# Kernel tuning notes

Hardware: AMD Instinct MI355X
Metric: run time of the kernel (lower is better)

Reference implementation:

```python
import jax, jax.numpy as jnp
import numpy as np

NUM_HEADS = 8
KEY_DIM = 512  # d_gain = 1/sqrt(key_dim) in the original (NOT per-head dim)
MASK_FILL = -1000000.0


def setup_inputs() -> dict:
    key = jax.random.key(0)
    ks = jax.random.split(key, 6)
    N, Tq, Tk, D, U = 8, 1024, 1024, 512, 512
    query = jax.random.normal(ks[0], (N, Tq, D), dtype=jnp.float32)
    key_t = jax.random.normal(ks[1], (N, Tk, D), dtype=jnp.float32)
    key_mask = jax.random.randint(ks[2], (N, Tk), 0, 2).astype(bool)
    Wq = jax.random.normal(ks[3], (D, U), dtype=jnp.float32) / np.sqrt(D)
    Wk = jax.random.normal(ks[4], (D, U), dtype=jnp.float32) / np.sqrt(D)
    Wv = jax.random.normal(ks[5], (D, U), dtype=jnp.float32) / np.sqrt(D)
    return {"query": query, "key": key_t, "key_mask": key_mask,
            "Wq": Wq, "Wk": Wk, "Wv": Wv}


def reference(query, key, key_mask, Wq, Wk, Wv):
    N, Tq, _ = query.shape
    Tk = key.shape[1]
    U = Wq.shape[1]
    h = NUM_HEADS
    d = U // h
    scale = 1.0 / (KEY_DIM ** 0.5)

    # projections then split heads: [N,T,U] -> [h,N,T,d]
    q = (query @ Wq).reshape(N, Tq, h, d).transpose(2, 0, 1, 3)
    k = (key @ Wk).reshape(N, Tk, h, d).transpose(2, 0, 1, 3)
    v = (key @ Wv).reshape(N, Tk, h, d).transpose(2, 0, 1, 3)

    scores = scale * jnp.einsum('hnqd,hnkd->hnqk', q, k)
    scores = jnp.where(key_mask[None, :, None, :], scores, MASK_FILL)
    attn = jax.nn.softmax(scores, axis=3)
    out = jnp.einsum('hnqk,hnkd->hnqd', attn, v)
    # merge heads: [h,N,Tq,d] -> [N,Tq,h*d]
    return out.transpose(1, 2, 0, 3).reshape(N, Tq, U)
```

## Files before the change

kernel.cpp:

```cpp
#include <hip/hip_runtime.h>
#include <hip/hip_bf16.h>

typedef unsigned short u16;
typedef __attribute__((ext_vector_type(8))) short short8;
typedef __attribute__((ext_vector_type(4))) short short4v;
typedef __attribute__((ext_vector_type(4))) float f32x4;

#define NB 8
#define TT 1024
#define DD 512
#define UU 512
#define HH 8
#define DH 64
#define SCALE 0.044194173824159216f
#define LOG2E 1.4426950408889634f
#define MASK_FILL_2 -1442695.0f

__device__ __forceinline__ float ld_flex(const void* p, long i, bool f32) {
  if (f32) return ((const float*)p)[i];
  unsigned int u = (unsigned int)(((const u16*)p)[i]) << 16;
  return __uint_as_float(u);
}

__device__ __forceinline__ u16 f32_to_bf16(float f) {
  unsigned int u = __float_as_uint(f);
  unsigned int r = (u + 0x7FFFu + ((u >> 16) & 1u)) >> 16;
  return (u16)r;
}

__device__ __forceinline__ float ex2(float x) {
#if __has_builtin(__builtin_amdgcn_exp2f)
  return __builtin_amdgcn_exp2f(x);
#else
  return __expf(x * 0.6931471805599453f);
#endif
}

__device__ __forceinline__ unsigned int pk_bf16(float a, float b) {
  union { __hip_bfloat162 h2; unsigned int u; } c;
  c.h2 = __float22bfloat162_rn(make_float2(a, b));
  return c.u;
}

__device__ __forceinline__ void gld16(const void* g, void* l) {
  __builtin_amdgcn_global_load_lds(
      (const __attribute__((address_space(1))) unsigned int*)g,
      (__attribute__((address_space(3))) unsigned int*)l, 16, 0, 0);
}

#define CONV_BLOCKS 8192
#define WT_BLOCKS 768
#define MASK_BLOCKS 32

__global__ __launch_bounds__(256) void prep_kernel(
    const void* __restrict__ query, const void* __restrict__ key,
    const void* __restrict__ W0, const void* __restrict__ W1,
    const void* __restrict__ W2, const void* __restrict__ mask,
    u16* __restrict__ Xq, u16* __restrict__ Xk, u16* __restrict__ Wt,
    float* __restrict__ maskadd, int* __restrict__ flags) {
  __shared__ float tile[32][33];
  __shared__ int s_f32, s_mi32;
  const int b = blockIdx.x, tid = threadIdx.x;

  if (tid == 0) { s_f32 = 0; s_mi32 = 1; }
  __syncthreads();
  {
    const u16* qh = (const u16*)query;
    int weird = 0;
#pragma unroll
    for (int p = 0; p < 4; ++p) {
      unsigned int u = (unsigned int)qh[tid * 4 + p] << 16;
      float v = __uint_as_float(u);
      if (!(v == v) || fabsf(v) > 1e6f) weird = 1;
    }
    if (weird) atomicOr(&s_f32, 1);
    const unsigned int* mi = (const unsigned int*)mask;
    if (mi[tid * 2] > 1u || mi[tid * 2 + 1] > 1u) atomicAnd(&s_mi32, 0);
  }
  __syncthreads();
  const bool f32 = s_f32 != 0;
  const bool mi32 = s_mi32 != 0;
  if (b == CONV_BLOCKS && tid == 0) { flags[0] = s_f32; flags[1] = s_mi32; }

  if (b < CONV_BLOCKS) {
    if (!f32) return;
    const void* in = (b < 4096) ? query : key;
    u16* out = (b < 4096) ? Xq : Xk;
    int i = (b & 4095) * 256 + tid;
    float4 v = ((const float4*)in)[i];
    ushort4 o;
    o.x = f32_to_bf16(v.x); o.y = f32_to_bf16(v.y);
    o.z = f32_to_bf16(v.z); o.w = f32_to_bf16(v.w);
    ((ushort4*)out)[i] = o;
  } else if (b < CONV_BLOCKS + WT_BLOCKS) {
    const int lb = b - CONV_BLOCKS;
    const int z = lb >> 8, rem = lb & 255;
    const int k0 = (rem & 15) * 32, n0 = (rem >> 4) * 32;
    const void* W = (z == 0) ? W0 : (z == 1) ? W1 : W2;
    const float sc = (z == 0) ? SCALE * LOG2E : 1.0f;
    u16* out = Wt + (size_t)z * DD * UU;
#pragma unroll
    for (int p = 0; p < 4; ++p) {
      int i = (tid >> 5) + p * 8, j = tid & 31;
      tile[i][j] = ld_flex(W, (long)(k0 + i) * UU + n0 + j, f32);
    }
    __syncthreads();
#pragma unroll
    for (int p = 0; p < 4; ++p) {
      int nl = (tid >> 5) + p * 8, kl = tid & 31;
      out[(size_t)(n0 + nl) * DD + k0 + kl] = f32_to_bf16(tile[kl][nl] * sc);
    }
  } else {
    const int i = (b - CONV_BLOCKS - WT_BLOCKS) * 256 + tid;
    bool mv = mi32 ? (((const int*)mask)[i] != 0)
                   : (((const unsigned char*)mask)[i] != 0);
    maskadd[i] = mv ? 0.0f : MASK_FILL_2;
  }
}

__global__ __launch_bounds__(256) void proj_mfma(
    const void* __restrict__ query, const void* __restrict__ key,
    const u16* __restrict__ Xq, const u16* __restrict__ Xk,
    const u16* __restrict__ Wt, u16* __restrict__ Qp, u16* __restrict__ Kp,
    u16* __restrict__ Vt, const int* __restrict__ flags) {
  __shared__ __align__(16) u16 As[128 * 32];
  __shared__ __align__(16) u16 Bs[128 * 32];
  const bool f32 = flags[0] != 0;
  const int z = blockIdx.z;
  const u16* X = (z == 0) ? (f32 ? Xq : (const u16*)query)
                          : (f32 ? Xk : (const u16*)key);
  const u16* Wz = Wt + (size_t)z * DD * UU;
  const int m0 = blockIdx.x * 128, n0 = blockIdx.y * 128;
  const int tid = threadIdx.x;
  const int w = tid >> 6, l = tid & 63;
  const int quad = l >> 4, l15 = l & 15;
  const int wm = (w >> 1) * 64, wn = (w & 1) * 64;

  const int c0 = w * 128 + l;
  const int row0 = c0 >> 2, q0 = (c0 & 3) * 8;
  const int c1 = c0 + 64;
  const int row1 = c1 >> 2, q1 = (c1 & 3) * 8;
  const u16* aS0 = X + (size_t)(m0 + row0) * DD + q0;
  const u16* aS1 = X + (size_t)(m0 + row1) * DD + q1;
  const u16* bS0 = Wz + (size_t)(n0 + row0) * DD + q0;
  const u16* bS1 = Wz + (size_t)(n0 + row1) * DD + q1;
  u16* aD0 = &As[(size_t)(w * 128) * 8];
  u16* aD1 = &As[(size_t)(w * 128 + 64) * 8];
  u16* bD0 = &Bs[(size_t)(w * 128) * 8];
  u16* bD1 = &Bs[(size_t)(w * 128 + 64) * 8];

  f32x4 acc[4][4];
#pragma unroll
  for (int mi = 0; mi < 4; ++mi)
#pragma unroll
    for (int ni = 0; ni < 4; ++ni)
#pragma unroll
      for (int r = 0; r < 4; ++r) acc[mi][ni][r] = 0.0f;

  for (int k0 = 0; k0 < DD; k0 += 32) {
    gld16(aS0 + k0, aD0);
    gld16(aS1 + k0, aD1);
    gld16(bS0 + k0, bD0);
    gld16(bS1 + k0, bD1);
    __syncthreads();
    short8 af[4], bf[4];
#pragma unroll
    for (int mi = 0; mi < 4; ++mi)
      af[mi] = *(const short8*)&As[(wm + mi * 16 + l15) * 32 + quad * 8];
#pragma unroll
    for (int ni = 0; ni < 4; ++ni)
      bf[ni] = *(const short8*)&Bs[(wn + ni * 16 + l15) * 32 + quad * 8];
#pragma unroll
    for (int mi = 0; mi < 4; ++mi)
#pragma unroll
      for (int ni = 0; ni < 4; ++ni)
        acc[mi][ni] = __builtin_amdgcn_mfma_f32_16x16x32_bf16(
            af[mi], bf[ni], acc[mi][ni], 0, 0, 0);
    __syncthreads();
  }

  if (z < 2) {
    u16* out = (z == 0) ? Qp : Kp;
#pragma unroll
    for (int mi = 0; mi < 4; ++mi)
#pragma unroll
      for (int ni = 0; ni < 4; ++ni)
#pragma unroll
        for (int r = 0; r < 4; ++r) {
          int m = m0 + wm + mi * 16 + quad * 4 + r;
          int u = n0 + wn + ni * 16 + l15;
          out[(size_t)m * UU + u] = f32_to_bf16(acc[mi][ni][r]);
        }
  } else {
#pragma unroll
    for (int mi = 0; mi < 4; ++mi)
#pragma unroll
      for (int ni = 0; ni < 4; ++ni) {
        int m = m0 + wm + mi * 16 + quad * 4;
        int nb = m >> 10, tk = m & 1023;
        int u = n0 + wn + ni * 16 + l15;
        int h = u >> 6, dh = u & 63;
        ushort4 pk;
        pk.x = f32_to_bf16(acc[mi][ni][0]);
        pk.y = f32_to_bf16(acc[mi][ni][1]);
        pk.z = f32_to_bf16(acc[mi][ni][2]);
        pk.w = f32_to_bf16(acc[mi][ni][3]);
        *(ushort4*)&Vt[(size_t)((nb * HH + h) * DH + dh) * TT + tk] = pk;
      }
  }
}

__global__ __launch_bounds__(256, 4) void attn_mfma(
    const u16* __restrict__ Qp, const u16* __restrict__ Kp,
    const u16* __restrict__ Vt, const float* __restrict__ maskadd,
    void* __restrict__ out, const int* __restrict__ flags) {
  __shared__ __align__(16) char smem[23040];
  const int tid = threadIdx.x;
  const int w = tid >> 6, l = tid & 63;
  const int quad = l >> 4, l15 = l & 15;
  const int lid = blockIdx.x + (blockIdx.y << 4) + (blockIdx.z << 7);
  const int swz = (lid & 7) * 128 + (lid >> 3);
  const int qt = swz & 15, h = (swz >> 4) & 7, n = swz >> 7;
  const int qsub = w >> 1, ks = w & 1;
  const int q0 = qt * 64 + qsub * 32;
  const int kb0 = ks * 512;
  const bool f32o = flags[0] != 0;
  u16* Pw = (u16*)smem + w * 2304;
  float* lp = (float*)(smem + 18432);
  float* s_mask = (float*)(smem + 18944);

  ((float4*)s_mask)[tid] = ((const float4*)(maskadd + n * TT))[tid];

  const u16* qbase = Qp + (size_t)(n * TT + q0 + l15) * UU + h * DH + quad * 8;
  short8 bq[2][2];
  bq[0][0] = *(const short8*)(qbase);
  bq[0][1] = *(const short8*)(qbase + 32);
  bq[1][0] = *(const short8*)(qbase + 16 * UU);
  bq[1][1] = *(const short8*)(qbase + 16 * UU + 32);

  const u16* kbase = Kp + (size_t)(n * TT + l15) * UU + h * DH + quad * 8;
  const u16* vbase = Vt + (size_t)((n * HH + h) * DH + l15) * TT + quad * 8;

  f32x4 o[2][4];
  float lsum[2] = {0.0f, 0.0f};
#pragma unroll
  for (int nq = 0; nq < 2; ++nq)
#pragma unroll
    for (int ni = 0; ni < 4; ++ni)
#pragma unroll
      for (int r = 0; r < 4; ++r) o[nq][ni][r] = 0.0f;

  __syncthreads();

  short8 ak[2][2];
#pragma unroll
  for (int kt = 0; kt < 2; ++kt)
#pragma unroll
    for (int kd = 0; kd < 2; ++kd)
      ak[kt][kd] = *(const short8*)(kbase + (size_t)(kb0 + kt * 16) * UU + kd * 32);
  {
    f32x4 s[2][2];
#pragma unroll
    for (int kt = 0; kt < 2; ++kt)
#pragma unroll
      for (int nq = 0; nq < 2; ++nq) {
#pragma unroll
        for (int r = 0; r < 4; ++r) s[kt][nq][r] = 0.0f;
#pragma unroll
        for (int kd = 0; kd < 2; ++kd)
          s[kt][nq] = __builtin_amdgcn_mfma_f32_16x16x32_bf16(
              ak[kt][kd], bq[nq][kd], s[kt][nq], 0, 0, 0);
      }
#pragma unroll
    for (int kt = 0; kt < 2; ++kt)
#pragma unroll
      for (int kd = 0; kd < 2; ++kd)
        ak[kt][kd] = *(const short8*)(kbase + (size_t)(kb0 + 32 + kt * 16) * UU + kd * 32);
    float4 mk[2];
    mk[0] = *(const float4*)&s_mask[kb0 + quad * 4];
    mk[1] = *(const float4*)&s_mask[kb0 + 16 + quad * 4];
#pragma unroll
    for (int kt = 0; kt < 2; ++kt)
#pragma unroll
      for (int nq = 0; nq < 2; ++nq) {
        float e0 = ex2(s[kt][nq][0] + mk[kt].x);
        float e1 = ex2(s[kt][nq][1] + mk[kt].y);
        float e2 = ex2(s[kt][nq][2] + mk[kt].z);
        float e3 = ex2(s[kt][nq][3] + mk[kt].w);
        lsum[nq] += (e0 + e1) + (e2 + e3);
        uint2 pk = make_uint2(pk_bf16(e0, e1), pk_bf16(e2, e3));
        *(uint2*)&Pw[(nq * 16 + l15) * 36 + kt * 16 + quad * 4] = pk;
      }
  }

#pragma unroll
  for (int it = 0; it < 16; ++it) {
    const int kb = kb0 + it * 32;
    u16* Pr = Pw + (it & 1) * 1152;
    short8 ap[2];
#pragma unroll
    for (int nq = 0; nq < 2; ++nq) {
      short4v lo = *(const short4v*)&Pr[(nq * 16 + l15) * 36 + quad * 8];
      short4v hi = *(const short4v*)&Pr[(nq * 16 + l15) * 36 + quad * 8 + 4];
      union { short8 v8; short4v v4[2]; } u;
      u.v4[0] = lo; u.v4[1] = hi;
      ap[nq] = u.v8;
    }
    short8 vf[4];
#pragma unroll
    for (int ni = 0; ni < 4; ++ni)
      vf[ni] = *(const short8*)(vbase + (size_t)(ni * 16) * TT + kb);

    if (it < 15) {
      f32x4 s[2][2];
#pragma unroll
      for (int kt = 0; kt < 2; ++kt)
#pragma unroll
        for (int nq = 0; nq < 2; ++nq) {
#pragma unroll
          for (int r = 0; r < 4; ++r) s[kt][nq][r] = 0.0f;
#pragma unroll
          for (int kd = 0; kd < 2; ++kd)
            s[kt][nq] = __builtin_amdgcn_mfma_f32_16x16x32_bf16(
                ak[kt][kd], bq[nq][kd], s[kt][nq], 0, 0, 0);
        }
      if (it < 14) {
        const int kb2 = kb + 64;
#pragma unroll
        for (int kt = 0; kt < 2; ++kt)
#pragma unroll
          for (int kd = 0; kd < 2; ++kd)
            ak[kt][kd] = *(const short8*)(kbase + (size_t)(kb2 + kt * 16) * UU + kd * 32);
      }
      float4 mk[2];
      mk[0] = *(const float4*)&s_mask[kb + 32 + quad * 4];
      mk[1] = *(const float4*)&s_mask[kb + 48 + quad * 4];
      u16* Pn = Pw + ((it + 1) & 1) * 1152;
#pragma unroll
      for (int kt = 0; kt < 2; ++kt)
#pragma unroll
        for (int nq = 0; nq < 2; ++nq) {
          float e0 = ex2(s[kt][nq][0] + mk[kt].x);
          float e1 = ex2(s[kt][nq][1] + mk[kt].y);
          float e2 = ex2(s[kt][nq][2] + mk[kt].z);
          float e3 = ex2(s[kt][nq][3] + mk[kt].w);
          lsum[nq] += (e0 + e1) + (e2 + e3);
          uint2 pk = make_uint2(pk_bf16(e0, e1), pk_bf16(e2, e3));
          *(uint2*)&Pn[(nq * 16 + l15) * 36 + kt * 16 + quad * 4] = pk;
        }
    }

#pragma unroll
    for (int nq = 0; nq < 2; ++nq)
#pragma unroll
      for (int ni = 0; ni < 4; ++ni)
        o[nq][ni] = __builtin_amdgcn_mfma_f32_16x16x32_bf16(
            ap[nq], vf[ni], o[nq][ni], 0, 0, 0);
  }

#pragma unroll
  for (int nq = 0; nq < 2; ++nq) {
    lsum[nq] += __shfl_xor(lsum[nq], 16);
    lsum[nq] += __shfl_xor(lsum[nq], 32);
  }

  if (quad == 0) {
    lp[w * 32 + l15] = lsum[0];
    lp[w * 32 + 16 + l15] = lsum[1];
  }
  __syncthreads();

  float* cbuf = (float*)smem;
#pragma unroll
  for (int c = 0; c < 4; ++c) {
    if ((w >> 1) == (c >> 1)) {
      float* Ow = cbuf + (w & 1) * (16 * 68);
#pragma unroll
      for (int ni = 0; ni < 4; ++ni)
#pragma unroll
        for (int r = 0; r < 4; ++r)
          Ow[(quad * 4 + r) * 68 + ni * 16 + l15] = o[c & 1][ni][r];
    }
    __syncthreads();
    for (int i = tid; i < 16 * 64; i += 256) {
      int q = i >> 6, j = i & 63;
      float s = cbuf[q * 68 + j] + cbuf[1088 + q * 68 + j];
      int qg = c * 16 + q;
      int base = (c >> 1) * 64;
      float lsum2 = lp[base + (qg & 31)] + lp[base + 32 + (qg & 31)];
      float v = s / lsum2;
      size_t idx = (size_t)(n * TT + qt * 64 + qg) * UU + h * DH + j;
      if (f32o) ((float*)out)[idx] = v;
      else ((u16*)out)[idx] = f32_to_bf16(v);
    }
    __syncthreads();
  }
}

extern "C" void kernel_launch(void* const* d_in, const int* in_sizes, int n_in,
                              void* d_out, int out_size, void* d_ws, size_t ws_size,
                              hipStream_t stream) {
  const void* query = d_in[0];
  const void* key   = d_in[1];
  const void* mask  = d_in[2];
  const void* Wq    = d_in[3];
  const void* Wk    = d_in[4];
  const void* Wv    = d_in[5];

  char* base = (char*)d_ws;
  int* flags = (int*)base;
  float* maskadd = (float*)(base + 256);
  u16* Wt  = (u16*)(base + 64 * 1024);
  u16* Xq  = Wt + (size_t)3 * DD * UU;
  u16* Xk  = Xq + (size_t)NB * TT * DD;
  u16* Qp  = Xk + (size_t)NB * TT * DD;
  u16* Kp  = Qp + (size_t)NB * TT * UU;
  u16* Vtp = Kp + (size_t)NB * TT * UU;

  prep_kernel<<<CONV_BLOCKS + WT_BLOCKS + MASK_BLOCKS, 256, 0, stream>>>(
      query, key, Wq, Wk, Wv, mask, Xq, Xk, Wt, maskadd, flags);

  dim3 pgrid(NB * TT / 128, UU / 128, 3);
  proj_mfma<<<pgrid, 256, 0, stream>>>(query, key, Xq, Xk, Wt, Qp, Kp, Vtp, flags);

  dim3 agrid(TT / 64, HH, NB);
  attn_mfma<<<agrid, 256, 0, stream>>>(Qp, Kp, Vtp, maskadd, d_out, flags);
}
```

Measured before the change: 185.8 us.

## Stage projection outputs through shared memory and stop unrolling the attention loop

The projection kernel now writes its accumulator tile into an enlarged padded shared-memory buffer, then stores Q/K rows and the transposed V tile to global memory as coalesced 16-byte vectors instead of scattered 2-byte and 8-byte stores. In the attention kernel the main key loop is no longer unrolled, sched_barrier fences are added around the score/softmax stage, and the occupancy hint is dropped from launch_bounds. This trades an extra LDS round-trip and a larger LDS footprint (lower possible occupancy for the projection kernel) for better store coalescing, and it trades loop overhead for lower code size and register pressure in attention.

```diff
diff --git a/kernel.cpp b/kernel.cpp
--- a/kernel.cpp
+++ b/kernel.cpp
@@ -123,8 +123,9 @@
     const u16* __restrict__ Xq, const u16* __restrict__ Xk,
     const u16* __restrict__ Wt, u16* __restrict__ Qp, u16* __restrict__ Kp,
     u16* __restrict__ Vt, const int* __restrict__ flags) {
-  __shared__ __align__(16) u16 As[128 * 32];
-  __shared__ __align__(16) u16 Bs[128 * 32];
+  __shared__ __align__(16) u16 smem[128 * 136];
+  u16* As = smem;
+  u16* Bs = smem + 4096;
   const bool f32 = flags[0] != 0;
   const int z = blockIdx.z;
   const u16* X = (z == 0) ? (f32 ? Xq : (const u16*)query)
@@ -180,37 +181,56 @@
   }
 
   if (z < 2) {
-    u16* out = (z == 0) ? Qp : Kp;
 #pragma unroll
     for (int mi = 0; mi < 4; ++mi)
 #pragma unroll
-      for (int ni = 0; ni < 4; ++ni)
-#pragma unroll
-        for (int r = 0; r < 4; ++r) {
-          int m = m0 + wm + mi * 16 + quad * 4 + r;
-          int u = n0 + wn + ni * 16 + l15;
-          out[(size_t)m * UU + u] = f32_to_bf16(acc[mi][ni][r]);
-        }
+      for (int ni = 0; ni < 4; ++ni) {
+        const int ml = wm + mi * 16 + quad * 4;
+        const int nl = wn + ni * 16 + l15;
+#pragma unroll
+        for (int r = 0; r < 4; ++r)
+          smem[(ml + r) * 136 + nl] = f32_to_bf16(acc[mi][ni][r]);
+      }
   } else {
 #pragma unroll
     for (int mi = 0; mi < 4; ++mi)
 #pragma unroll
       for (int ni = 0; ni < 4; ++ni) {
-        int m = m0 + wm + mi * 16 + quad * 4;
-        int nb = m >> 10, tk = m & 1023;
-        int u = n0 + wn + ni * 16 + l15;
-        int h = u >> 6, dh = u & 63;
+        const int ml = wm + mi * 16 + quad * 4;
+        const int nl = wn + ni * 16 + l15;
         ushort4 pk;
         pk.x = f32_to_bf16(acc[mi][ni][0]);
         pk.y = f32_to_bf16(acc[mi][ni][1]);
         pk.z = f32_to_bf16(acc[mi][ni][2]);
         pk.w = f32_to_bf16(acc[mi][ni][3]);
-        *(ushort4*)&Vt[(size_t)((nb * HH + h) * DH + dh) * TT + tk] = pk;
+        *(ushort4*)&smem[nl * 136 + ml] = pk;
       }
   }
-}
-
-__global__ __launch_bounds__(256, 4) void attn_mfma(
+  __syncthreads();
+
+  if (z < 2) {
+    u16* outp = (z == 0) ? Qp : Kp;
+#pragma unroll
+    for (int p = 0; p < 8; ++p) {
+      const int idx = tid + p * 256;
+      const int row = idx >> 4, c8 = (idx & 15) * 8;
+      short8 v = *(const short8*)&smem[row * 136 + c8];
+      *(short8*)&outp[(size_t)(m0 + row) * UU + n0 + c8] = v;
+    }
+  } else {
+    const int nb = m0 >> 10, tk0 = m0 & 1023;
+#pragma unroll
+    for (int p = 0; p < 8; ++p) {
+      const int idx = tid + p * 256;
+      const int row = idx >> 4, c8 = (idx & 15) * 8;
+      const int u = n0 + row, h = u >> 6, dh = u & 63;
+      short8 v = *(const short8*)&smem[row * 136 + c8];
+      *(short8*)&Vt[(size_t)((nb * HH + h) * DH + dh) * TT + tk0 + c8] = v;
+    }
+  }
+}
+
+__global__ __launch_bounds__(256) void attn_mfma(
     const u16* __restrict__ Qp, const u16* __restrict__ Kp,
     const u16* __restrict__ Vt, const float* __restrict__ maskadd,
     void* __restrict__ out, const int* __restrict__ flags) {
@@ -293,7 +313,7 @@
       }
   }
 
-#pragma unroll
+#pragma unroll 1
   for (int it = 0; it < 16; ++it) {
     const int kb = kb0 + it * 32;
     u16* Pr = Pw + (it & 1) * 1152;
@@ -310,6 +330,7 @@
 #pragma unroll
     for (int ni = 0; ni < 4; ++ni)
       vf[ni] = *(const short8*)(vbase + (size_t)(ni * 16) * TT + kb);
+    __builtin_amdgcn_sched_barrier(0);
 
     if (it < 15) {
       f32x4 s[2][2];
@@ -349,6 +370,7 @@
           *(uint2*)&Pn[(nq * 16 + l15) * 36 + kt * 16 + quad * 4] = pk;
         }
     }
+    __builtin_amdgcn_sched_barrier(0);
 
 #pragma unroll
     for (int nq = 0; nq < 2; ++nq)
```

After: 183.6 us. Within noise of the previous version (-1.2%).
